# Kernel tuning notes

Measured on AMD Instinct MI355X. Metric: run time of the kernel, lower is better.

## Reference

```python
import jax, jax.numpy as jnp
import numpy as np

B, L, N, FA, FB, D, OUT, R, T = 128, 128, 6, 39, 10, 200, 1, 3, 2
MB = 256  # num bonds per molecule
NEG = -9e8


def setup_inputs():
    key = jax.random.key(0)
    ks = iter(jax.random.split(key, 64))
    def rn(shape, sc=0.05):
        return jax.random.normal(next(ks), shape, dtype=jnp.float32) * sc
    inp = {}
    inp['atom_list'] = jax.random.normal(next(ks), (B, L, FA), dtype=jnp.float32)
    inp['bond_list'] = jax.random.normal(next(ks), (B, MB, FB), dtype=jnp.float32)
    inp['atom_degree_list'] = jax.random.randint(next(ks), (B, L, N), 0, L, dtype=jnp.int32)
    inp['bond_degree_list'] = jax.random.randint(next(ks), (B, L, N), 0, MB, dtype=jnp.int32)
    inp['atom_mask'] = jnp.ones((B, L), dtype=jnp.float32)
    # parameters (torch Linear: y = x @ W + b with W stored here as [in, out])
    inp['W_atom'] = rn((FA, D)); inp['b_atom'] = rn((D,))
    inp['W_nei'] = rn((FA + FB, D)); inp['b_nei'] = rn((D,))
    inp['W_align'] = rn((R, 2 * D, 1)); inp['b_align'] = rn((R, 1))
    inp['W_attend'] = rn((R, D, D)); inp['b_attend'] = rn((R, D))
    # GRUCell weights, torch layout [3D, D], gate order r,z,n
    inp['Wih'] = rn((R, 3 * D, D)); inp['Whh'] = rn((R, 3 * D, D))
    inp['bih'] = rn((R, 3 * D)); inp['bhh'] = rn((R, 3 * D))
    inp['W_mol_align'] = rn((2 * D, 1)); inp['b_mol_align'] = rn((1,))
    inp['W_mol_attend'] = rn((D, D)); inp['b_mol_attend'] = rn((D,))
    inp['mWih'] = rn((3 * D, D)); inp['mWhh'] = rn((3 * D, D))
    inp['mbih'] = rn((3 * D,)); inp['mbhh'] = rn((3 * D,))
    inp['W_metric'] = rn((2 * D, D)); inp['b_metric'] = rn((D,))
    inp['W_out'] = rn((D, OUT)); inp['b_out'] = rn((OUT,))
    return inp


def _gather(feat, idx):
    # feat [B, M, F], idx [B, L, N] -> [B, L, N, F]
    b, l, n = idx.shape
    g = jnp.take_along_axis(feat, idx.reshape(b, l * n)[..., None], axis=1)
    return g.reshape(b, l, n, feat.shape[-1])


def _gru(x, h, Wih, Whh, bih, bhh):
    gi = x @ Wih.T + bih
    gh = h @ Whh.T + bhh
    ir, iz, inn = jnp.split(gi, 3, axis=-1)
    hr, hz, hn = jnp.split(gh, 3, axis=-1)
    r = jax.nn.sigmoid(ir + hr)
    z = jax.nn.sigmoid(iz + hz)
    n = jnp.tanh(inn + r * hn)
    return (1.0 - z) * n + z * h


def reference(atom_list, bond_list, atom_degree_list, bond_degree_list, atom_mask,
              W_atom, b_atom, W_nei, b_nei, W_align, b_align, W_attend, b_attend,
              Wih, Whh, bih, bhh, W_mol_align, b_mol_align, W_mol_attend, b_mol_attend,
              mWih, mWhh, mbih, mbhh, W_metric, b_metric, W_out, b_out):
    lrelu = jax.nn.leaky_relu
    b, l, _ = atom_list.shape
    atom_feature = lrelu(atom_list @ W_atom + b_atom)          # [B,L,D]
    atom_nei = _gather(atom_list, atom_degree_list)            # [B,L,N,FA]
    bond_nei = _gather(bond_list, bond_degree_list)            # [B,L,N,FB]
    nei = lrelu(jnp.concatenate([atom_nei, bond_nei], -1) @ W_nei + b_nei)  # [B,L,N,D]

    pad = (atom_degree_list == l - 1)
    attend_mask = (~pad).astype(jnp.float32)[..., None]        # [B,L,N,1]
    softmax_mask = jnp.where(pad, NEG, 0.0)[..., None]         # [B,L,N,1]

    h = atom_feature
    cur = atom_feature
    for r in range(R):
        if r > 0:
            nei = _gather(cur, atom_degree_list)
        exp = jnp.broadcast_to(cur[:, :, None, :], nei.shape)
        align = lrelu(jnp.concatenate([exp, nei], -1) @ W_align[r] + b_align[r])
        w = jax.nn.softmax(align + softmax_mask, axis=-2) * attend_mask
        trans = nei @ W_attend[r] + b_attend[r]
        ctx = jax.nn.elu(jnp.sum(w * trans, axis=-2))          # [B,L,D]
        h = _gru(ctx.reshape(-1, D), h.reshape(-1, D), Wih[r], Whh[r], bih[r], bhh[r]).reshape(b, l, D)
        cur = jax.nn.relu(h)

    am = atom_mask[..., None]                                   # [B,L,1]
    mol_feature = jnp.sum(cur * am, axis=-2)                    # [B,D]
    act_mol = jax.nn.relu(mol_feature)
    mol_softmax_mask = jnp.where(am == 0.0, NEG, 0.0)           # [B,L,1]
    for _ in range(T):
        exp = jnp.broadcast_to(act_mol[:, None, :], cur.shape)
        score = lrelu(jnp.concatenate([exp, cur], -1) @ W_mol_align + b_mol_align)
        w = jax.nn.softmax(score + mol_softmax_mask, axis=-2) * am
        trans = cur @ W_mol_attend + b_mol_attend
        ctx = jax.nn.elu(jnp.sum(w * trans, axis=-2))           # [B,D]
        mol_feature = _gru(ctx, mol_feature, mWih, mWhh, mbih, mbhh)
        act_mol = jax.nn.relu(mol_feature)

    dd = jnp.float32(R - 2)  # leaked python loop var `d` in the original
    feat = jnp.concatenate([mol_feature, mol_feature + dd], -1)
    return (feat @ W_metric + b_metric) @ W_out + b_out


if __name__ == '__main__':
    out = reference(**setup_inputs())
    print(out.shape)
```

## Files before the change

### kernel.cpp

```cpp
#include <hip/hip_runtime.h>
#include <hip/hip_bf16.h>
#include <math.h>
#include <string.h>

#define B_ 128
#define L_ 128
#define N_ 6
#define FA_ 39
#define FB_ 10
#define D_ 200
#define MB_ 256
#define R_ 3
#define T_ 2
#define NEGV -9e8f
#define BL_ (B_*L_)
#define BLD_ (BL_*D_)
#define G3D_ (3*D_)
#define FP32TAG 0x3F800000u
#define KP 416
#define NP 896
#define KC 224
#define NC 256

typedef __hip_bfloat16 bf16;
typedef __attribute__((ext_vector_type(8))) short short8;
typedef __attribute__((ext_vector_type(4))) float f32x4;

__device__ __forceinline__ float b2f(const bf16 x){ return __bfloat162float(x); }
__device__ __forceinline__ unsigned short f2b(float v){ bf16 t = __float2bfloat16(v); return *reinterpret_cast<unsigned short*>(&t); }
__device__ __forceinline__ float bu2f(unsigned short u){ unsigned x = ((unsigned)u)<<16; float f; memcpy(&f,&x,4); return f; }
__device__ __forceinline__ float lreluf(float x){ return x>=0.f ? x : 0.01f*x; }
__device__ __forceinline__ float eluf(float x){ return x>0.f ? x : expm1f(x); }
__device__ __forceinline__ float sigmf(float x){ return 1.f/(1.f+expf(-x)); }

#define NSEG 14
struct CvtArgs { const void* src[NSEG]; int ofs[NSEG+1]; };

#define PREPB_N (R_*NP*KP)
#define PREPW_N (R_*NC*KC)
#define PREPM_N (D_*G3D_)
#define PREPT_N 40000
#define PREPE_N 80000
#define PREPQ_N (B_*MB_*D_)
#define CONV_N 23989

struct PrepArgs {
    CvtArgs cvt;
    const void *Wih, *Whh, *Watt, *mWih, *mWhh, *Wmt, *Wme;
    const void *bond, *Wnei, *atom, *Watom, *batom, *bnei, *Walign;
    float* conv;
    unsigned short *B2t, *WatT, *mTi, *mTh, *Wmt16, *Wme16, *Q16, *XH, *P16;
    float *s1, *tb;
    const unsigned* amtag;
    int ew_total;
    int ew_blocks;
};

__device__ __forceinline__ float ldd(const void* p, size_t i, bool f32){
    return f32 ? ((const float*)p)[i] : b2f(((const bf16*)p)[i]);
}

__global__ void __launch_bounds__(256) k_prep(PrepArgs A){
    bool f32 = (*A.amtag == FP32TAG);
    int bid = blockIdx.x;
    if (bid < A.ew_blocks){
        int i = bid*256 + (int)threadIdx.x;
        if (i >= A.ew_total) return;
        if (i < CONV_N){
            int s = 0;
            while (i >= A.cvt.ofs[s+1]) s++;
            A.conv[i] = ldd(A.cvt.src[s], i - A.cvt.ofs[s], f32);
            return;
        }
        int i2 = i - CONV_N;
        if (i2 < PREPB_N){
            int kk = i2 % KP;
            int rest = i2 / KP;
            int n = rest % NP;
            int r = rest / NP;
            float v = 0.f;
            if (kk < 200){
                if (n < 600) v = ldd(A.Wih, ((size_t)(r*G3D_ + n))*D_ + kk, f32);
            } else if (kk < 400){
                int j = -1;
                if (n < 400) j = n;
                else if (n >= 600 && n < 800) j = n - 200;
                if (j >= 0) v = ldd(A.Whh, ((size_t)(r*G3D_ + j))*D_ + (kk-200), f32);
            }
            A.B2t[i2] = f2b(v);
            return;
        }
        int i3 = i2 - PREPB_N;
        if (i3 < PREPW_N){
            int kk = i3 % KC;
            int rest = i3 / KC;
            int n = rest % NC;
            int r = rest / NC;
            float v = 0.f;
            if (kk < 200 && n < 200) v = ldd(A.Watt, ((size_t)r*D_ + kk)*D_ + n, f32);
            A.WatT[i3] = f2b(v);
            return;
        }
        int i4 = i3 - PREPW_N;
        if (i4 < PREPM_N){
            int j = i4 % G3D_, k = i4 / G3D_;
            size_t si = (size_t)j*D_ + k;
            A.mTi[i4] = f2b(ldd(A.mWih, si, f32));
            A.mTh[i4] = f2b(ldd(A.mWhh, si, f32));
            return;
        }
        int i5 = i4 - PREPM_N;
        if (i5 < PREPT_N){
            A.Wmt16[i5] = f2b(ldd(A.Wmt, i5, f32));
            return;
        }
        int i6 = i5 - PREPT_N;
        if (i6 < PREPE_N){
            A.Wme16[i6] = f2b(ldd(A.Wme, i6, f32));
            return;
        }
        int i7 = i6 - PREPE_N;
        {
            int d = i7 % D_;
            int row = i7 / D_;
            float acc = 0.f;
            if (f32){
                const float* br = (const float*)A.bond + (size_t)row*FB_;
                const float* Wb = (const float*)A.Wnei;
                #pragma unroll
                for (int k=0;k<FB_;k++) acc += br[k] * Wb[(FA_+k)*D_ + d];
            } else {
                const bf16* br = (const bf16*)A.bond + (size_t)row*FB_;
                const bf16* Wb = (const bf16*)A.Wnei;
                #pragma unroll
                for (int k=0;k<FB_;k++) acc += b2f(br[k]) * b2f(Wb[(FA_+k)*D_ + d]);
            }
            A.Q16[i7] = f2b(acc);
            return;
        }
    }
    int ib = bid - A.ew_blocks;
    int wv = threadIdx.x >> 6, lane = threadIdx.x & 63;
    int al = ib*4 + wv;
    float areg[FA_];
    if (f32){
        const float* a = (const float*)A.atom + (size_t)al*FA_;
        #pragma unroll
        for (int k=0;k<FA_;k++) areg[k] = a[k];
    } else {
        const bf16* a = (const bf16*)A.atom + (size_t)al*FA_;
        #pragma unroll
        for (int k=0;k<FA_;k++) areg[k] = b2f(a[k]);
    }
    float a1 = 0.f, a2 = 0.f;
    if (f32){
        const float* WA = (const float*)A.Watom;
        const float* WN = (const float*)A.Wnei;
        const float* ba = (const float*)A.batom;
        const float* bn = (const float*)A.bnei;
        const float* Wl = (const float*)A.Walign;
        for (int d = lane; d < D_; d += 64){
            float acc1 = ba[d], acc2 = bn[d];
            #pragma unroll
            for (int k=0;k<FA_;k++){
                acc1 += areg[k] * WA[k*D_ + d];
                acc2 += areg[k] * WN[k*D_ + d];
            }
            float v = lreluf(acc1);
            A.XH[(size_t)al*KP + 200 + d] = f2b(v);
            A.P16[(size_t)al*D_ + d] = f2b(acc2);
            a1 += v * Wl[d];
            a2 += v * Wl[D_ + d];
        }
    } else {
        const bf16* WA = (const bf16*)A.Watom;
        const bf16* WN = (const bf16*)A.Wnei;
        const bf16* ba = (const bf16*)A.batom;
        const bf16* bn = (const bf16*)A.bnei;
        const bf16* Wl = (const bf16*)A.Walign;
        for (int d = lane; d < D_; d += 64){
            float acc1 = b2f(ba[d]), acc2 = b2f(bn[d]);
            #pragma unroll
            for (int k=0;k<FA_;k++){
                acc1 += areg[k] * b2f(WA[k*D_ + d]);
                acc2 += areg[k] * b2f(WN[k*D_ + d]);
            }
            float v = lreluf(acc1);
            A.XH[(size_t)al*KP + 200 + d] = f2b(v);
            A.P16[(size_t)al*D_ + d] = f2b(acc2);
            a1 += v * b2f(Wl[d]);
            a2 += v * b2f(Wl[D_ + d]);
        }
    }
    if (lane < 16) A.XH[(size_t)al*KP + 400 + lane] = 0;
    for (int o=32;o>0;o>>=1){ a1 += __shfl_xor(a1,o); a2 += __shfl_xor(a2,o); }
    if (lane==0){ A.s1[al] = a1; A.tb[al] = a2; }
}

__global__ void __launch_bounds__(256) k_attn(
        const unsigned short* __restrict__ cur16,
        const float* __restrict__ s1, const float* __restrict__ tb,
        const int* __restrict__ adl, const int* __restrict__ bdl,
        const unsigned short* __restrict__ P16, const unsigned short* __restrict__ Q16,
        const float* __restrict__ W_align, const float* __restrict__ b_align, int r,
        unsigned short* __restrict__ wnei, float* __restrict__ wsum){
    int bid = blockIdx.x;
    int mol = bid & (B_-1), chunk = bid >> 7;
    int wv = threadIdx.x >> 6, lane = threadIdx.x & 63;
    int al = mol*L_ + chunk*4 + wv;
    __shared__ float s_nei[4][N_][D_];

    int idxn[N_]; bool pad[N_];
    for (int n=0;n<N_;n++){ idxn[n] = adl[al*N_ + n]; pad[n] = (idxn[n] == L_-1); }

    float s2[N_];
    if (r == 0){
        for (int j = lane; j < N_*D_; j += 64){
            int n = j / D_, d = j - n*D_;
            int bd = bdl[al*N_ + n];
            float acc = bu2f(P16[((size_t)mol*L_ + idxn[n])*D_ + d])
                      + bu2f(Q16[((size_t)mol*MB_ + bd)*D_ + d]);
            s_nei[wv][n][d] = lreluf(acc);
        }
        const float* Wab = W_align + D_;
        for (int n=0;n<N_;n++){
            float acc = 0.f;
            for (int d=lane; d<D_; d+=64) acc += s_nei[wv][n][d] * Wab[d];
            for (int o=32;o>0;o>>=1) acc += __shfl_xor(acc,o);
            s2[n] = acc;
        }
    } else {
        float tmp = 0.f;
        if (lane < N_) tmp = tb[mol*L_ + idxn[lane]];
        for (int n=0;n<N_;n++) s2[n] = __shfl(tmp, n);
    }

    float s1v = s1[al];
    float bav = b_align[r];
    float a[N_]; float mx = -1e30f;
    for (int n=0;n<N_;n++){
        float v = lreluf(s1v + s2[n] + bav);
        if (pad[n]) v += NEGV;
        a[n] = v; mx = fmaxf(mx, v);
    }
    float w[N_]; float se = 0.f;
    for (int n=0;n<N_;n++){ float e = expf(a[n]-mx); w[n]=e; se += e; }
    float inv = 1.f/se; float wsv = 0.f;
    for (int n=0;n<N_;n++){ w[n] = pad[n] ? 0.f : w[n]*inv; wsv += w[n]; }

    if (r == 0){
        for (int d=lane; d<D_; d+=64){
            float acc = 0.f;
            #pragma unroll
            for (int n=0;n<N_;n++) acc += w[n] * s_nei[wv][n][d];
            wnei[(size_t)al*KC + d] = f2b(acc);
        }
    } else {
        for (int d=lane; d<D_; d+=64){
            float acc = 0.f;
            #pragma unroll
            for (int n=0;n<N_;n++) acc += w[n] * bu2f(cur16[((size_t)mol*L_ + idxn[n])*KC + d]);
            wnei[(size_t)al*KC + d] = f2b(acc);
        }
    }
    if (lane < 24) wnei[(size_t)al*KC + 200 + lane] = 0;
    if (lane==0) wsum[al] = wsv;
}

__global__ void __launch_bounds__(256) k_ctxmfma(const unsigned short* __restrict__ Wn,
        const float* __restrict__ wsum, const unsigned short* __restrict__ WatT,
        const float* __restrict__ bias, int r, unsigned short* __restrict__ XH){
    __shared__ unsigned short As[128][40];
    __shared__ unsigned short Bs[64][40];
    int tid = threadIdx.x;
    int m0 = ((int)blockIdx.x & 127) * 128;
    int n0 = ((int)blockIdx.x >> 7) * 64;
    const unsigned short* Bt = WatT + (size_t)r*NC*KC;
    int lane = tid & 63, wv = tid >> 6;
    int quad = lane >> 4, lm = lane & 15;
    f32x4 acc[2][4];
    #pragma unroll
    for (int a=0;a<2;a++)
        #pragma unroll
        for (int b=0;b<4;b++) acc[a][b] = (f32x4){0.f,0.f,0.f,0.f};
    for (int ks = 0; ks < 7; ks++){
        int r0_ = tid >> 2, c0 = (tid & 3) * 8;
        int r1_ = (tid + 256) >> 2, c1 = ((tid + 256) & 3) * 8;
        uint4 a0 = *(const uint4*)&Wn[(size_t)(m0 + r0_)*KC + ks*32 + c0];
        uint4 a1 = *(const uint4*)&Wn[(size_t)(m0 + r1_)*KC + ks*32 + c1];
        uint4 b0 = *(const uint4*)&Bt[(size_t)(n0 + (tid >> 2))*KC + ks*32 + (tid & 3)*8];
        __syncthreads();
        *(uint4*)&As[r0_][c0] = a0;
        *(uint4*)&As[r1_][c1] = a1;
        *(uint4*)&Bs[tid >> 2][(tid & 3)*8] = b0;
        __syncthreads();
        short8 av0 = *(const short8*)&As[wv*32 + lm][quad*8];
        short8 av1 = *(const short8*)&As[wv*32 + 16 + lm][quad*8];
        #pragma unroll
        for (int ns=0; ns<4; ns++){
            short8 bv = *(const short8*)&Bs[ns*16 + lm][quad*8];
            acc[0][ns] = __builtin_amdgcn_mfma_f32_16x16x32_bf16(av0, bv, acc[0][ns], 0,0,0);
            acc[1][ns] = __builtin_amdgcn_mfma_f32_16x16x32_bf16(av1, bv, acc[1][ns], 0,0,0);
        }
    }
    #pragma unroll
    for (int ms=0; ms<2; ms++)
      #pragma unroll
      for (int ns=0; ns<4; ns++){
        int n = n0 + ns*16 + lm;
        if (n < 200){
            float bv = bias[r*D_ + n];
            #pragma unroll
            for (int i=0;i<4;i++){
                int row = m0 + wv*32 + ms*16 + quad*4 + i;
                float v = acc[ms][ns][i] + wsum[row]*bv;
                XH[(size_t)row*KP + n] = f2b(eluf(v));
            }
        }
      }
}

__global__ void __launch_bounds__(256) k_gemm(const unsigned short* __restrict__ XH,
        const unsigned short* __restrict__ B2t, unsigned short* __restrict__ C, int r){
    __shared__ unsigned short As[128][40];
    __shared__ unsigned short Bs[128][40];
    int tid = threadIdx.x;
    int m0 = ((int)blockIdx.x & 127) * 128;
    int n0 = ((int)blockIdx.x >> 7) * 128;
    const unsigned short* Bt = B2t + (size_t)r*NP*KP;
    int lane = tid & 63, wv = tid >> 6;
    int quad = lane >> 4, lm = lane & 15;
    f32x4 acc[2][8];
    #pragma unroll
    for (int a=0;a<2;a++)
        #pragma unroll
        for (int b=0;b<8;b++) acc[a][b] = (f32x4){0.f,0.f,0.f,0.f};
    for (int ks = 0; ks < 13; ks++){
        int r0_ = tid >> 2, c0 = (tid & 3) * 8;
        int r1_ = (tid + 256) >> 2, c1 = ((tid + 256) & 3) * 8;
        uint4 a0 = *(const uint4*)&XH[(size_t)(m0 + r0_)*KP + ks*32 + c0];
        uint4 a1 = *(const uint4*)&XH[(size_t)(m0 + r1_)*KP + ks*32 + c1];
        uint4 b0 = *(const uint4*)&Bt[(size_t)(n0 + r0_)*KP + ks*32 + c0];
        uint4 b1 = *(const uint4*)&Bt[(size_t)(n0 + r1_)*KP + ks*32 + c1];
        __syncthreads();
        *(uint4*)&As[r0_][c0] = a0;
        *(uint4*)&As[r1_][c1] = a1;
        *(uint4*)&Bs[r0_][c0] = b0;
        *(uint4*)&Bs[r1_][c1] = b1;
        __syncthreads();
        short8 av0 = *(const short8*)&As[wv*32 + lm][quad*8];
        short8 av1 = *(const short8*)&As[wv*32 + 16 + lm][quad*8];
        #pragma unroll
        for (int ns=0; ns<8; ns++){
            short8 bv = *(const short8*)&Bs[ns*16 + lm][quad*8];
            acc[0][ns] = __builtin_amdgcn_mfma_f32_16x16x32_bf16(av0, bv, acc[0][ns], 0,0,0);
            acc[1][ns] = __builtin_amdgcn_mfma_f32_16x16x32_bf16(av1, bv, acc[1][ns], 0,0,0);
        }
    }
    #pragma unroll
    for (int ms=0; ms<2; ms++)
      #pragma unroll
      for (int ns=0; ns<8; ns++)
        #pragma unroll
        for (int i=0;i<4;i++){
            int row = m0 + wv*32 + ms*16 + quad*4 + i;
            C[(size_t)row*NP + n0 + ns*16 + lm] = f2b(acc[ms][ns][i]);
        }
}

__global__ void __launch_bounds__(256) k_gru2(const unsigned short* __restrict__ C,
        unsigned short* __restrict__ XH, unsigned short* __restrict__ cur16,
        const float* __restrict__ bih, const float* __restrict__ bhh,
        const float* __restrict__ W_align, const float* __restrict__ Wma, int r,
        float* __restrict__ s1, float* __restrict__ tb, float* __restrict__ curdot){
    int wv = threadIdx.x >> 6, lane = threadIdx.x & 63;
    int al = blockIdx.x*4 + wv;
    size_t base = (size_t)al*NP;
    const float* bi = bih + r*G3D_;
    const float* bh = bhh + r*G3D_;
    const float* Wa = W_align + (r+1)*2*D_;
    bool last = (r == R_-1);
    float a1 = 0.f, a2 = 0.f;
    for (int j = lane; j < D_; j += 64){
        float rsum = bu2f(C[base + j]);
        float zsum = bu2f(C[base + 200 + j]);
        float gin  = bu2f(C[base + 400 + j]);
        float ghn  = bu2f(C[base + 600 + j]);
        float rr = sigmf(rsum + bi[j] + bh[j]);
        float zz = sigmf(zsum + bi[D_+j] + bh[D_+j]);
        float nn = tanhf(gin + bi[2*D_+j] + rr*(ghn + bh[2*D_+j]));
        size_t hx = (size_t)al*KP + 200 + j;
        float hv = bu2f(XH[hx]);
        float hn = (1.f-zz)*nn + zz*hv;
        XH[hx] = f2b(hn);
        float cv = fmaxf(hn, 0.f);
        cur16[(size_t)al*KC + j] = f2b(cv);
        if (last){
            a1 += cv * Wma[D_+j];
        } else {
            a1 += cv * Wa[j];
            a2 += cv * Wa[D_+j];
        }
    }
    if (lane < 24) cur16[(size_t)al*KC + 200 + lane] = 0;
    for (int o=32;o>0;o>>=1){ a1 += __shfl_xor(a1,o); a2 += __shfl_xor(a2,o); }
    if (lane==0){
        if (last) curdot[al] = a1;
        else { s1[al] = a1; tb[al] = a2; }
    }
}

__device__ __forceinline__ float brSum(float v, float* s_red){
    for (int o=32;o>0;o>>=1) v += __shfl_xor(v,o);
    int lane = threadIdx.x & 63, wid = threadIdx.x >> 6;
    __syncthreads();
    if (lane==0) s_red[wid] = v;
    __syncthreads();
    float r = 0.f;
    int nw = blockDim.x >> 6;
    for (int i=0;i<nw;i++) r += s_red[i];
    return r;
}

__device__ __forceinline__ float brMax(float v, float* s_red){
    for (int o=32;o>0;o>>=1) v = fmaxf(v, __shfl_xor(v,o));
    int lane = threadIdx.x & 63, wid = threadIdx.x >> 6;
    __syncthreads();
    if (lane==0) s_red[wid] = v;
    __syncthreads();
    float r = s_red[0];
    int nw = blockDim.x >> 6;
    for (int i=1;i<nw;i++) r = fmaxf(r, s_red[i]);
    return r;
}

__global__ void __launch_bounds__(512) k_mol(const unsigned short* __restrict__ cur16,
    const float* __restrict__ curdot, const float* __restrict__ atom_mask,
    const float* __restrict__ Wma, const float* __restrict__ bma,
    const unsigned short* __restrict__ Wmt16, const float* __restrict__ bmt,
    const unsigned short* __restrict__ mTi, const unsigned short* __restrict__ mTh,
    const float* __restrict__ mbih, const float* __restrict__ mbhh,
    const unsigned short* __restrict__ Wme16, const float* __restrict__ bme,
    const float* __restrict__ Wout, const float* __restrict__ bout,
    void* __restrict__ out, const unsigned* __restrict__ amtag){
    int b = blockIdx.x, tid = threadIdx.x;
    int dq = tid & 255, cq = tid >> 8;
    __shared__ unsigned short s_cur[L_*KC];
    __shared__ float s_am[L_], s_neg[L_], s_cd[L_], s_w[L_];
    __shared__ float s_mf[D_], s_act[D_], s_wc[D_], s_ctx[D_];
    __shared__ float s_gi[G3D_], s_gh[G3D_];
    __shared__ float s_part[2][256];
    __shared__ float s_red[8];
    const uint4* src = (const uint4*)(cur16 + (size_t)b*L_*KC);
    for (int i = tid; i < L_*KC/8; i += 512) ((uint4*)s_cur)[i] = src[i];
    if (tid < L_){
        float am = atom_mask[b*L_ + tid];
        s_am[tid] = am;
        s_neg[tid] = (am == 0.f) ? NEGV : 0.f;
        s_cd[tid] = curdot[b*L_ + tid];
    }
    __syncthreads();
    {
        float a0 = 0.f, a1 = 0.f;
        if (dq < D_)
            for (int l=cq*64; l<cq*64+64; l+=2){
                a0 += bu2f(s_cur[l*KC + dq]) * s_am[l];
                a1 += bu2f(s_cur[(l+1)*KC + dq]) * s_am[l+1];
            }
        s_part[cq][dq] = a0 + a1;
        __syncthreads();
        if (tid < D_){
            float v = s_part[0][tid] + s_part[1][tid];
            s_mf[tid] = v; s_act[tid] = fmaxf(v, 0.f);
        }
        __syncthreads();
    }
    float bma0 = bma[0];
    for (int t=0;t<T_;t++){
        float p = (tid < D_) ? s_act[tid] * Wma[tid] : 0.f;
        float s1v = brSum(p, s_red);
        float sc = (tid < L_) ? (lreluf(s1v + s_cd[tid] + bma0) + s_neg[tid]) : -1e30f;
        float mx = brMax(sc, s_red);
        float e = (tid < L_) ? expf(sc - mx) : 0.f;
        float se = brSum(e, s_red);
        float wv_ = (tid < L_) ? e/se*s_am[tid] : 0.f;
        if (tid < L_) s_w[tid] = wv_;
        float wsm = brSum(wv_, s_red);
        __syncthreads();
        {
            float a0 = 0.f, a1 = 0.f;
            if (dq < D_)
                for (int l=cq*64; l<cq*64+64; l+=2){
                    a0 += s_w[l] * bu2f(s_cur[l*KC + dq]);
                    a1 += s_w[l+1] * bu2f(s_cur[(l+1)*KC + dq]);
                }
            s_part[cq][dq] = a0 + a1;
            __syncthreads();
            if (tid < D_) s_wc[tid] = s_part[0][tid] + s_part[1][tid];
            __syncthreads();
        }
        {
            float a0 = 0.f, a1 = 0.f;
            if (dq < D_)
                for (int k=cq*100; k<cq*100+100; k+=2){
                    a0 += s_wc[k] * bu2f(Wmt16[(size_t)k*D_ + dq]);
                    a1 += s_wc[k+1] * bu2f(Wmt16[(size_t)(k+1)*D_ + dq]);
                }
            s_part[cq][dq] = a0 + a1;
            __syncthreads();
            if (tid < D_)
                s_ctx[tid] = eluf(s_part[0][tid] + s_part[1][tid] + wsm * bmt[tid]);
            __syncthreads();
        }
        for (int j=tid; j<G3D_; j+=512){
            float ai0=0.f, ai1=0.f, ai2=0.f, ai3=0.f;
            float ah0=0.f, ah1=0.f, ah2=0.f, ah3=0.f;
            for (int k=0;k<D_;k+=4){
                ai0 += s_ctx[k]   * bu2f(mTi[(size_t)k*G3D_ + j]);
                ai1 += s_ctx[k+1] * bu2f(mTi[(size_t)(k+1)*G3D_ + j]);
                ai2 += s_ctx[k+2] * bu2f(mTi[(size_t)(k+2)*G3D_ + j]);
                ai3 += s_ctx[k+3] * bu2f(mTi[(size_t)(k+3)*G3D_ + j]);
                ah0 += s_mf[k]    * bu2f(mTh[(size_t)k*G3D_ + j]);
                ah1 += s_mf[k+1]  * bu2f(mTh[(size_t)(k+1)*G3D_ + j]);
                ah2 += s_mf[k+2]  * bu2f(mTh[(size_t)(k+2)*G3D_ + j]);
                ah3 += s_mf[k+3]  * bu2f(mTh[(size_t)(k+3)*G3D_ + j]);
            }
            s_gi[j] = (ai0+ai1)+(ai2+ai3); s_gh[j] = (ah0+ah1)+(ah2+ah3);
        }
        __syncthreads();
        if (tid < D_){
            int d = tid;
            float rr = sigmf(s_gi[d] + mbih[d] + s_gh[d] + mbhh[d]);
            float zz = sigmf(s_gi[D_+d] + mbih[D_+d] + s_gh[D_+d] + mbhh[D_+d]);
            float nn = tanhf(s_gi[2*D_+d] + mbih[2*D_+d] + rr*(s_gh[2*D_+d] + mbhh[2*D_+d]));
            float nm = (1.f-zz)*nn + zz*s_mf[d];
            s_mf[d] = nm; s_act[d] = fmaxf(nm, 0.f);
        }
        __syncthreads();
    }
    const float dd = (float)(R_ - 2);
    {
        float a0 = 0.f, a1 = 0.f;
        if (dq < D_)
            for (int k=cq*100; k<cq*100+100; k+=2){
                float mf0 = s_mf[k], mf1 = s_mf[k+1];
                a0 += mf0 * bu2f(Wme16[(size_t)k*D_ + dq])
                    + (mf0 + dd) * bu2f(Wme16[(size_t)(D_+k)*D_ + dq]);
                a1 += mf1 * bu2f(Wme16[(size_t)(k+1)*D_ + dq])
                    + (mf1 + dd) * bu2f(Wme16[(size_t)(D_+k+1)*D_ + dq]);
            }
        s_part[cq][dq] = a0 + a1;
        __syncthreads();
        float p = 0.f;
        if (tid < D_)
            p = (s_part[0][tid] + s_part[1][tid] + bme[tid]) * Wout[tid];
        float o = brSum(p, s_red);
        if (tid==0){
            o += bout[0];
            if (*amtag == FP32TAG) ((float*)out)[b] = o;
            else ((bf16*)out)[b] = __float2bfloat16(o);
        }
    }
}

extern "C" void kernel_launch(void* const* d_in, const int* in_sizes, int n_in,
                              void* d_out, int out_size, void* d_ws, size_t ws_size,
                              hipStream_t stream) {
    const int* adl = (const int*)d_in[2];
    const int* bdl = (const int*)d_in[3];
    const unsigned* amtag = (const unsigned*)d_in[4];

    static const int srcidx[NSEG] = {4,9,10,12,15,16,17,18,20,23,24,26,27,28};
    static const int segsz[NSEG]  = {16384,1200,3,600,1800,1800,400,1,200,600,600,200,200,1};
    CvtArgs ca;
    int ofs[NSEG+1]; ofs[0] = 0;
    for (int i=0;i<NSEG;i++){ ca.src[i] = d_in[srcidx[i]]; ca.ofs[i] = ofs[i]; ofs[i+1] = ofs[i] + segsz[i]; }
    ca.ofs[NSEG] = ofs[NSEG];

    float* ws   = (float*)d_ws;
    float* conv = ws;
    unsigned short* XH    = (unsigned short*)(conv + 24000);
    unsigned short* B2t   = XH + (size_t)BL_*KP;
    unsigned short* WatT  = B2t + PREPB_N;
    unsigned short* mTi   = WatT + PREPW_N;
    unsigned short* mTh   = mTi + PREPM_N;
    unsigned short* Wmt16 = mTh + PREPM_N;
    unsigned short* Wme16 = Wmt16 + PREPT_N;
    unsigned short* cur16 = Wme16 + PREPE_N;
    unsigned short* creg  = cur16 + (size_t)BL_*KC;
    unsigned short* C = creg;
    unsigned short* wnei = creg;
    unsigned short* Q16  = creg + (size_t)BL_*KC;
    unsigned short* P16  = Q16 + PREPQ_N;
    float* s1     = (float*)(creg + (size_t)BL_*NP);
    float* tb     = s1 + BL_;
    float* wsum   = tb + BL_;
    float* curdot = wsum + BL_;

    const float* c_amask = conv + ofs[0];
    const float* c_Walign= conv + ofs[1];
    const float* c_balign= conv + ofs[2];
    const float* c_batt  = conv + ofs[3];
    const float* c_bih   = conv + ofs[4];
    const float* c_bhh   = conv + ofs[5];
    const float* c_Wma   = conv + ofs[6];
    const float* c_bma   = conv + ofs[7];
    const float* c_bmt   = conv + ofs[8];
    const float* c_mbih  = conv + ofs[9];
    const float* c_mbhh  = conv + ofs[10];
    const float* c_bme   = conv + ofs[11];
    const float* c_Wout  = conv + ofs[12];
    const float* c_bout  = conv + ofs[13];

    PrepArgs A;
    A.cvt = ca;
    A.Wih = d_in[13]; A.Whh = d_in[14]; A.Watt = d_in[11];
    A.mWih = d_in[21]; A.mWhh = d_in[22]; A.Wmt = d_in[19]; A.Wme = d_in[25];
    A.bond = d_in[1]; A.Wnei = d_in[7]; A.atom = d_in[0];
    A.Watom = d_in[5]; A.batom = d_in[6]; A.bnei = d_in[8]; A.Walign = d_in[9];
    A.conv = conv;
    A.B2t = B2t; A.WatT = WatT; A.mTi = mTi; A.mTh = mTh;
    A.Wmt16 = Wmt16; A.Wme16 = Wme16; A.Q16 = Q16; A.XH = XH; A.P16 = P16;
    A.s1 = s1; A.tb = tb;
    A.amtag = amtag;
    A.ew_total = CONV_N + PREPB_N + PREPW_N + PREPM_N + PREPT_N + PREPE_N + PREPQ_N;
    A.ew_blocks = (A.ew_total + 255) / 256;
    int grid = A.ew_blocks + BL_/4;

    k_prep<<<grid, 256, 0, stream>>>(A);

    for (int r=0; r<R_; r++){
        k_attn<<<BL_/4, 256, 0, stream>>>(cur16, s1, tb, adl, bdl, P16, Q16,
                                          c_Walign, c_balign, r, wnei, wsum);
        k_ctxmfma<<<(BL_/128)*(NC/64), 256, 0, stream>>>(wnei, wsum, WatT, c_batt, r, XH);
        k_gemm<<<(BL_/128)*(NP/128), 256, 0, stream>>>(XH, B2t, C, r);
        k_gru2<<<BL_/4, 256, 0, stream>>>(C, XH, cur16, c_bih, c_bhh,
                                          c_Walign, c_Wma, r, s1, tb, curdot);
    }

    k_mol<<<B_, 512, 0, stream>>>(cur16, curdot, c_amask, c_Wma, c_bma, Wmt16, c_bmt,
                                  mTi, mTh, c_mbih, c_mbhh, Wme16, c_bme, c_Wout, c_bout,
                                  d_out, amtag);
}
```

Before: 494.1 us.

## Compute initial atom and bond projections with an MFMA GEMM kernel

Replaces the scalar per-atom FMA loops and the per-element bond projection (Q16) in the prep kernel with a packed bf16 A/B layout and a new MFMA-based GEMM kernel, k_initmm, that produces XH, P16 and Q16 together. The s1 align dot product moves into k_attn for round 0, where it is read back from XH. This removes a large scalar compute phase (B*MB*D elements times FB) in exchange for an extra launch and extra packing writes. It also adds bf16 rounding of the inputs before the projection.

```diff
diff --git a/kernel.cpp b/kernel.cpp
--- a/kernel.cpp
+++ b/kernel.cpp
@@ -14,7 +14,6 @@
 #define T_ 2
 #define NEGV -9e8f
 #define BL_ (B_*L_)
-#define BLD_ (BL_*D_)
 #define G3D_ (3*D_)
 #define FP32TAG 0x3F800000u
 #define KP 416
@@ -41,19 +40,20 @@
 #define PREPM_N (D_*G3D_)
 #define PREPT_N 40000
 #define PREPE_N 80000
-#define PREPQ_N (B_*MB_*D_)
 #define CONV_N 23989
+#define XHPAD_N (BL_*16)
+#define AROWS (BL_ + B_*MB_)
+#define A_N (AROWS*64)
+#define BI_N (448*64)
 
 struct PrepArgs {
     CvtArgs cvt;
     const void *Wih, *Whh, *Watt, *mWih, *mWhh, *Wmt, *Wme;
-    const void *bond, *Wnei, *atom, *Watom, *batom, *bnei, *Walign;
+    const void *bond, *Wnei, *atom, *Watom;
     float* conv;
-    unsigned short *B2t, *WatT, *mTi, *mTh, *Wmt16, *Wme16, *Q16, *XH, *P16;
-    float *s1, *tb;
+    unsigned short *B2t, *WatT, *mTi, *mTh, *Wmt16, *Wme16, *XH, *A16, *Bi16;
     const unsigned* amtag;
     int ew_total;
-    int ew_blocks;
 };
 
 __device__ __forceinline__ float ldd(const void* p, size_t i, bool f32){
@@ -62,143 +62,156 @@
 
 __global__ void __launch_bounds__(256) k_prep(PrepArgs A){
     bool f32 = (*A.amtag == FP32TAG);
-    int bid = blockIdx.x;
-    if (bid < A.ew_blocks){
-        int i = bid*256 + (int)threadIdx.x;
-        if (i >= A.ew_total) return;
-        if (i < CONV_N){
-            int s = 0;
-            while (i >= A.cvt.ofs[s+1]) s++;
-            A.conv[i] = ldd(A.cvt.src[s], i - A.cvt.ofs[s], f32);
-            return;
-        }
-        int i2 = i - CONV_N;
-        if (i2 < PREPB_N){
-            int kk = i2 % KP;
-            int rest = i2 / KP;
-            int n = rest % NP;
-            int r = rest / NP;
-            float v = 0.f;
-            if (kk < 200){
-                if (n < 600) v = ldd(A.Wih, ((size_t)(r*G3D_ + n))*D_ + kk, f32);
-            } else if (kk < 400){
-                int j = -1;
-                if (n < 400) j = n;
-                else if (n >= 600 && n < 800) j = n - 200;
-                if (j >= 0) v = ldd(A.Whh, ((size_t)(r*G3D_ + j))*D_ + (kk-200), f32);
+    int i = blockIdx.x*256 + (int)threadIdx.x;
+    if (i >= A.ew_total) return;
+    if (i < CONV_N){
+        int s = 0;
+        while (i >= A.cvt.ofs[s+1]) s++;
+        A.conv[i] = ldd(A.cvt.src[s], i - A.cvt.ofs[s], f32);
+        return;
+    }
+    int i2 = i - CONV_N;
+    if (i2 < PREPB_N){
+        int kk = i2 % KP;
+        int rest = i2 / KP;
+        int n = rest % NP;
+        int r = rest / NP;
+        float v = 0.f;
+        if (kk < 200){
+            if (n < 600) v = ldd(A.Wih, ((size_t)(r*G3D_ + n))*D_ + kk, f32);
+        } else if (kk < 400){
+            int j = -1;
+            if (n < 400) j = n;
+            else if (n >= 600 && n < 800) j = n - 200;
+            if (j >= 0) v = ldd(A.Whh, ((size_t)(r*G3D_ + j))*D_ + (kk-200), f32);
+        }
+        A.B2t[i2] = f2b(v);
+        return;
+    }
+    int i3 = i2 - PREPB_N;
+    if (i3 < PREPW_N){
+        int kk = i3 % KC;
+        int rest = i3 / KC;
+        int n = rest % NC;
+        int r = rest / NC;
+        float v = 0.f;
+        if (kk < 200 && n < 200) v = ldd(A.Watt, ((size_t)r*D_ + kk)*D_ + n, f32);
+        A.WatT[i3] = f2b(v);
+        return;
+    }
+    int i4 = i3 - PREPW_N;
+    if (i4 < PREPM_N){
+        int j = i4 % G3D_, k = i4 / G3D_;
+        size_t si = (size_t)j*D_ + k;
+        A.mTi[i4] = f2b(ldd(A.mWih, si, f32));
+        A.mTh[i4] = f2b(ldd(A.mWhh, si, f32));
+        return;
+    }
+    int i5 = i4 - PREPM_N;
+    if (i5 < PREPT_N){
+        A.Wmt16[i5] = f2b(ldd(A.Wmt, i5, f32));
+        return;
+    }
+    int i6 = i5 - PREPT_N;
+    if (i6 < PREPE_N){
+        A.Wme16[i6] = f2b(ldd(A.Wme, i6, f32));
+        return;
+    }
+    int i7 = i6 - PREPE_N;
+    if (i7 < XHPAD_N){
+        int al = i7 >> 4, j = i7 & 15;
+        A.XH[(size_t)al*KP + 400 + j] = 0;
+        return;
+    }
+    int i8 = i7 - XHPAD_N;
+    if (i8 < A_N){
+        int row = i8 >> 6, k = i8 & 63;
+        float v = 0.f;
+        if (row < BL_){
+            if (k < FA_) v = ldd(A.atom, (size_t)row*FA_ + k, f32);
+        } else {
+            int rb = row - BL_;
+            if (k >= FA_ && k < FA_+FB_) v = ldd(A.bond, (size_t)rb*FB_ + (k-FA_), f32);
+        }
+        A.A16[i8] = f2b(v);
+        return;
+    }
+    int i9 = i8 - A_N;
+    if (i9 < BI_N){
+        int n = i9 >> 6, k = i9 & 63;
+        float v = 0.f;
+        if (n < 200){
+            if (k < FA_) v = ldd(A.Watom, (size_t)k*D_ + n, f32);
+        } else if (n < 400){
+            if (k < FA_+FB_) v = ldd(A.Wnei, (size_t)k*D_ + (n-200), f32);
+        }
+        A.Bi16[i9] = f2b(v);
+    }
+}
+
+__global__ void __launch_bounds__(256) k_initmm(const unsigned short* __restrict__ A16,
+        const unsigned short* __restrict__ Bi16,
+        const void* __restrict__ batom, const void* __restrict__ bnei,
+        unsigned short* __restrict__ XH, unsigned short* __restrict__ P16,
+        unsigned short* __restrict__ Q16, const unsigned* __restrict__ amtag){
+    __shared__ unsigned short As[128][40];
+    __shared__ unsigned short Bs[64][40];
+    bool f32 = (*amtag == FP32TAG);
+    int tid = threadIdx.x;
+    int mt = (int)blockIdx.x / 7, nt = (int)blockIdx.x % 7;
+    int m0 = mt*128, n0 = nt*64;
+    if (m0 >= BL_ && n0 + 64 <= 200) return;
+    int lane = tid & 63, wv = tid >> 6;
+    int quad = lane >> 4, lm = lane & 15;
+    f32x4 acc[2][4];
+    #pragma unroll
+    for (int a=0;a<2;a++)
+        #pragma unroll
+        for (int b=0;b<4;b++) acc[a][b] = (f32x4){0.f,0.f,0.f,0.f};
+    for (int ks = 0; ks < 2; ks++){
+        int r0_ = tid >> 2, c0 = (tid & 3) * 8;
+        int r1_ = (tid + 256) >> 2, c1 = ((tid + 256) & 3) * 8;
+        uint4 a0 = *(const uint4*)&A16[(size_t)(m0 + r0_)*64 + ks*32 + c0];
+        uint4 a1 = *(const uint4*)&A16[(size_t)(m0 + r1_)*64 + ks*32 + c1];
+        uint4 b0 = *(const uint4*)&Bi16[(size_t)(n0 + (tid >> 2))*64 + ks*32 + (tid & 3)*8];
+        __syncthreads();
+        *(uint4*)&As[r0_][c0] = a0;
+        *(uint4*)&As[r1_][c1] = a1;
+        *(uint4*)&Bs[tid >> 2][(tid & 3)*8] = b0;
+        __syncthreads();
+        short8 av0 = *(const short8*)&As[wv*32 + lm][quad*8];
+        short8 av1 = *(const short8*)&As[wv*32 + 16 + lm][quad*8];
+        #pragma unroll
+        for (int ns=0; ns<4; ns++){
+            short8 bv = *(const short8*)&Bs[ns*16 + lm][quad*8];
+            acc[0][ns] = __builtin_amdgcn_mfma_f32_16x16x32_bf16(av0, bv, acc[0][ns], 0,0,0);
+            acc[1][ns] = __builtin_amdgcn_mfma_f32_16x16x32_bf16(av1, bv, acc[1][ns], 0,0,0);
+        }
+    }
+    #pragma unroll
+    for (int ms=0; ms<2; ms++)
+      #pragma unroll
+      for (int ns=0; ns<4; ns++){
+        int n = n0 + ns*16 + lm;
+        #pragma unroll
+        for (int i=0;i<4;i++){
+            int row = m0 + wv*32 + ms*16 + quad*4 + i;
+            float v = acc[ms][ns][i];
+            if (row < BL_){
+                if (n < 200){
+                    XH[(size_t)row*KP + 200 + n] = f2b(lreluf(v + ldd(batom, n, f32)));
+                } else if (n < 400){
+                    P16[(size_t)row*D_ + (n-200)] = f2b(v + ldd(bnei, n-200, f32));
+                }
+            } else if (n >= 200 && n < 400){
+                Q16[(size_t)(row-BL_)*D_ + (n-200)] = f2b(v);
             }
-            A.B2t[i2] = f2b(v);
-            return;
-        }
-        int i3 = i2 - PREPB_N;
-        if (i3 < PREPW_N){
-            int kk = i3 % KC;
-            int rest = i3 / KC;
-            int n = rest % NC;
-            int r = rest / NC;
-            float v = 0.f;
-            if (kk < 200 && n < 200) v = ldd(A.Watt, ((size_t)r*D_ + kk)*D_ + n, f32);
-            A.WatT[i3] = f2b(v);
-            return;
-        }
-        int i4 = i3 - PREPW_N;
-        if (i4 < PREPM_N){
-            int j = i4 % G3D_, k = i4 / G3D_;
-            size_t si = (size_t)j*D_ + k;
-            A.mTi[i4] = f2b(ldd(A.mWih, si, f32));
-            A.mTh[i4] = f2b(ldd(A.mWhh, si, f32));
-            return;
-        }
-        int i5 = i4 - PREPM_N;
-        if (i5 < PREPT_N){
-            A.Wmt16[i5] = f2b(ldd(A.Wmt, i5, f32));
-            return;
-        }
-        int i6 = i5 - PREPT_N;
-        if (i6 < PREPE_N){
-            A.Wme16[i6] = f2b(ldd(A.Wme, i6, f32));
-            return;
-        }
-        int i7 = i6 - PREPE_N;
-        {
-            int d = i7 % D_;
-            int row = i7 / D_;
-            float acc = 0.f;
-            if (f32){
-                const float* br = (const float*)A.bond + (size_t)row*FB_;
-                const float* Wb = (const float*)A.Wnei;
-                #pragma unroll
-                for (int k=0;k<FB_;k++) acc += br[k] * Wb[(FA_+k)*D_ + d];
-            } else {
-                const bf16* br = (const bf16*)A.bond + (size_t)row*FB_;
-                const bf16* Wb = (const bf16*)A.Wnei;
-                #pragma unroll
-                for (int k=0;k<FB_;k++) acc += b2f(br[k]) * b2f(Wb[(FA_+k)*D_ + d]);
-            }
-            A.Q16[i7] = f2b(acc);
-            return;
-        }
-    }
-    int ib = bid - A.ew_blocks;
-    int wv = threadIdx.x >> 6, lane = threadIdx.x & 63;
-    int al = ib*4 + wv;
-    float areg[FA_];
-    if (f32){
-        const float* a = (const float*)A.atom + (size_t)al*FA_;
-        #pragma unroll
-        for (int k=0;k<FA_;k++) areg[k] = a[k];
-    } else {
-        const bf16* a = (const bf16*)A.atom + (size_t)al*FA_;
-        #pragma unroll
-        for (int k=0;k<FA_;k++) areg[k] = b2f(a[k]);
-    }
-    float a1 = 0.f, a2 = 0.f;
-    if (f32){
-        const float* WA = (const float*)A.Watom;
-        const float* WN = (const float*)A.Wnei;
-        const float* ba = (const float*)A.batom;
-        const float* bn = (const float*)A.bnei;
-        const float* Wl = (const float*)A.Walign;
-        for (int d = lane; d < D_; d += 64){
-            float acc1 = ba[d], acc2 = bn[d];
-            #pragma unroll
-            for (int k=0;k<FA_;k++){
-                acc1 += areg[k] * WA[k*D_ + d];
-                acc2 += areg[k] * WN[k*D_ + d];
-            }
-            float v = lreluf(acc1);
-            A.XH[(size_t)al*KP + 200 + d] = f2b(v);
-            A.P16[(size_t)al*D_ + d] = f2b(acc2);
-            a1 += v * Wl[d];
-            a2 += v * Wl[D_ + d];
-        }
-    } else {
-        const bf16* WA = (const bf16*)A.Watom;
-        const bf16* WN = (const bf16*)A.Wnei;
-        const bf16* ba = (const bf16*)A.batom;
-        const bf16* bn = (const bf16*)A.bnei;
-        const bf16* Wl = (const bf16*)A.Walign;
-        for (int d = lane; d < D_; d += 64){
-            float acc1 = b2f(ba[d]), acc2 = b2f(bn[d]);
-            #pragma unroll
-            for (int k=0;k<FA_;k++){
-                acc1 += areg[k] * b2f(WA[k*D_ + d]);
-                acc2 += areg[k] * b2f(WN[k*D_ + d]);
-            }
-            float v = lreluf(acc1);
-            A.XH[(size_t)al*KP + 200 + d] = f2b(v);
-            A.P16[(size_t)al*D_ + d] = f2b(acc2);
-            a1 += v * b2f(Wl[d]);
-            a2 += v * b2f(Wl[D_ + d]);
-        }
-    }
-    if (lane < 16) A.XH[(size_t)al*KP + 400 + lane] = 0;
-    for (int o=32;o>0;o>>=1){ a1 += __shfl_xor(a1,o); a2 += __shfl_xor(a2,o); }
-    if (lane==0){ A.s1[al] = a1; A.tb[al] = a2; }
+        }
+      }
 }
 
 __global__ void __launch_bounds__(256) k_attn(
-        const unsigned short* __restrict__ cur16,
+        const unsigned short* __restrict__ cur16, const unsigned short* __restrict__ XH,
         const float* __restrict__ s1, const float* __restrict__ tb,
         const int* __restrict__ adl, const int* __restrict__ bdl,
         const unsigned short* __restrict__ P16, const unsigned short* __restrict__ Q16,
@@ -214,6 +227,7 @@
     for (int n=0;n<N_;n++){ idxn[n] = adl[al*N_ + n]; pad[n] = (idxn[n] == L_-1); }
 
     float s2[N_];
+    float s1v;
     if (r == 0){
         for (int j = lane; j < N_*D_; j += 64){
             int n = j / D_, d = j - n*D_;
@@ -229,13 +243,17 @@
             for (int o=32;o>0;o>>=1) acc += __shfl_xor(acc,o);
             s2[n] = acc;
         }
+        float a1 = 0.f;
+        for (int d=lane; d<D_; d+=64) a1 += bu2f(XH[(size_t)al*KP + 200 + d]) * W_align[d];
+        for (int o=32;o>0;o>>=1) a1 += __shfl_xor(a1,o);
+        s1v = a1;
     } else {
         float tmp = 0.f;
         if (lane < N_) tmp = tb[mol*L_ + idxn[lane]];
         for (int n=0;n<N_;n++) s2[n] = __shfl(tmp, n);
-    }
-
-    float s1v = s1[al];
+        s1v = s1[al];
+    }
+
     float bav = b_align[r];
     float a[N_]; float mx = -1e30f;
     for (int n=0;n<N_;n++){
@@ -586,12 +604,14 @@
     unsigned short* mTh   = mTi + PREPM_N;
     unsigned short* Wmt16 = mTh + PREPM_N;
     unsigned short* Wme16 = Wmt16 + PREPT_N;
-    unsigned short* cur16 = Wme16 + PREPE_N;
+    unsigned short* Bi16  = Wme16 + PREPE_N;
+    unsigned short* cur16 = Bi16 + BI_N;
     unsigned short* creg  = cur16 + (size_t)BL_*KC;
     unsigned short* C = creg;
+    unsigned short* A16  = creg;
     unsigned short* wnei = creg;
     unsigned short* Q16  = creg + (size_t)BL_*KC;
-    unsigned short* P16  = Q16 + PREPQ_N;
+    unsigned short* P16  = Q16 + (size_t)B_*MB_*D_;
     float* s1     = (float*)(creg + (size_t)BL_*NP);
     float* tb     = s1 + BL_;
     float* wsum   = tb + BL_;
@@ -616,21 +636,20 @@
     A.cvt = ca;
     A.Wih = d_in[13]; A.Whh = d_in[14]; A.Watt = d_in[11];
     A.mWih = d_in[21]; A.mWhh = d_in[22]; A.Wmt = d_in[19]; A.Wme = d_in[25];
-    A.bond = d_in[1]; A.Wnei = d_in[7]; A.atom = d_in[0];
-    A.Watom = d_in[5]; A.batom = d_in[6]; A.bnei = d_in[8]; A.Walign = d_in[9];
+    A.bond = d_in[1]; A.Wnei = d_in[7]; A.atom = d_in[0]; A.Watom = d_in[5];
     A.conv = conv;
     A.B2t = B2t; A.WatT = WatT; A.mTi = mTi; A.mTh = mTh;
-    A.Wmt16 = Wmt16; A.Wme16 = Wme16; A.Q16 = Q16; A.XH = XH; A.P16 = P16;
-    A.s1 = s1; A.tb = tb;
+    A.Wmt16 = Wmt16; A.Wme16 = Wme16; A.XH = XH; A.A16 = A16; A.Bi16 = Bi16;
     A.amtag = amtag;
-    A.ew_total = CONV_N + PREPB_N + PREPW_N + PREPM_N + PREPT_N + PREPE_N + PREPQ_N;
-    A.ew_blocks = (A.ew_total + 255) / 256;
-    int grid = A.ew_blocks + BL_/4;
-
-    k_prep<<<grid, 256, 0, stream>>>(A);
+    A.ew_total = CONV_N + PREPB_N + PREPW_N + PREPM_N + PREPT_N + PREPE_N
+               + XHPAD_N + A_N + BI_N;
+
+    k_prep<<<(A.ew_total + 255)/256, 256, 0, stream>>>(A);
+    k_initmm<<<(AROWS/128)*7, 256, 0, stream>>>(A16, Bi16, d_in[6], d_in[8],
+                                                XH, P16, Q16, amtag);
 
     for (int r=0; r<R_; r++){
-        k_attn<<<BL_/4, 256, 0, stream>>>(cur16, s1, tb, adl, bdl, P16, Q16,
+        k_attn<<<BL_/4, 256, 0, stream>>>(cur16, XH, s1, tb, adl, bdl, P16, Q16,
                                           c_Walign, c_balign, r, wnei, wsum);
         k_ctxmfma<<<(BL_/128)*(NC/64), 256, 0, stream>>>(wnei, wsum, WatT, c_batt, r, XH);
         k_gemm<<<(BL_/128)*(NP/128), 256, 0, stream>>>(XH, B2t, C, r);
```

After: 454.5 us. 8.0% less time.
